# Performance work log

Measured on AMD Instinct MI355X. Metric: run time of the kernel, lower is better.

## Reference

```python
import jax, jax.numpy as jnp
import numpy as np

T_VALUES = [0.015, 0.06, 0.25, 1.0]
EPS = 1e-05
SR_OVER_HOP = 44100.0 / 512.0  # frames per second


def _s_values():
    t = np.asarray(T_VALUES, dtype=np.float32) * SR_OVER_HOP
    s = (np.sqrt(1.0 + 4.0 * t ** 2) - 1.0) / (2.0 * t ** 2)
    return jnp.asarray(s, dtype=jnp.float32)  # (n_s,)


def setup_inputs() -> dict:
    key = jax.random.key(0)
    k1, = jax.random.split(key, 1)
    B, F, T = 16, 128, 4096
    # non-negative energies (spectrogram magnitudes)
    x = jax.random.uniform(k1, (B, F, T), dtype=jnp.float32) * 10.0
    alpha_log = jnp.full((F,), float(np.log(0.8)), dtype=jnp.float32)
    delta_log = jnp.full((F,), float(np.log(10.0)), dtype=jnp.float32)
    r_log = jnp.full((F,), float(np.log(0.25)), dtype=jnp.float32)
    return {"x": x, "alpha_log": alpha_log, "delta_log": delta_log, "r_log": r_log}


def reference(x, alpha_log, delta_log, r_log):
    # x: (B, F, T)
    s = _s_values()                      # (n_s,)
    s_b = s[:, None, None]               # (n_s, 1, 1)
    B, F, T = x.shape
    n_s = s.shape[0]

    # Multi-rate EMA over time (first-order IIR), init with first frame.
    xs = jnp.moveaxis(x, -1, 0)          # (T, B, F)
    m0 = jnp.broadcast_to(xs[0][None], (n_s, B, F))

    def step(m, xt):
        m = (1.0 - s_b) * m + s_b * xt[None]  # (n_s, B, F)
        return m, m

    _, m_rest = jax.lax.scan(step, m0, xs[1:])          # (T-1, n_s, B, F)
    m_seq = jnp.concatenate([m0[None], m_rest], axis=0)  # (T, n_s, B, F)
    smoother = jnp.moveaxis(m_seq, 0, -1)                # (n_s, B, F, T)

    alpha = jnp.exp(alpha_log)[None, None, :, None]      # per band
    delta = jnp.exp(delta_log)[None, None, :, None]
    r = jnp.exp(r_log)[None, None, :, None]

    log_eps = jnp.log(jnp.asarray(EPS, dtype=x.dtype))
    smooth = jnp.exp(-alpha * (log_eps + jnp.log1p(smoother / EPS)))
    pcen = (x[None] * smooth + delta) ** r - delta ** r   # (n_s, B, F, T)
    return jnp.transpose(pcen, (1, 0, 2, 3))              # (B, n_s, F, T)
```

## Files before the change

kernel.cpp:

```cpp
#include <hip/hip_runtime.h>


#define EPS_C 1e-5f

__device__ __forceinline__ float fexp2(float v) { return __builtin_amdgcn_exp2f(v); }
__device__ __forceinline__ float flog2(float v) { return __builtin_amdgcn_logf(v); }
__device__ __forceinline__ float fpow(float a, float b) { return fexp2(b * flog2(a)); }
__device__ __forceinline__ float fexp(float v) { return fexp2(v * 1.44269504f); }

__global__ __launch_bounds__(1024)
void pcen_kernel(const float* __restrict__ x,
                 const float* __restrict__ alpha_log,
                 const float* __restrict__ delta_log,
                 const float* __restrict__ r_log,
                 float* __restrict__ out)
{
    const int row  = blockIdx.x;
    const int f    = row & 127;
    const int b    = row >> 7;
    const int tid  = threadIdx.x;
    const int lane = tid & 63;
    const int w    = tid >> 6;

    __shared__ float wq[4][16];
    __shared__ float sh_x0;

    const float4* __restrict__ xrow4 = (const float4*)(x + (size_t)row * 4096);
    float4 xv = xrow4[tid];
    if (tid == 0) sh_x0 = xv.x;

    const float Tv[4] = {0.015f, 0.06f, 0.25f, 1.0f};
    float s_arr[4], omn_arr[4];
#pragma unroll
    for (int i = 0; i < 4; ++i) {
        float t  = Tv[i] * 86.1328125f;
        float t2 = t * t;
        float s  = (__builtin_sqrtf(1.0f + 4.0f * t2) - 1.0f) / (2.0f * t2);
        s_arr[i]   = s;
        omn_arr[i] = 1.0f - s;
    }

    float qxv[4];
#pragma unroll
    for (int i = 0; i < 4; ++i) {
        const float s = s_arr[i], omn = omn_arr[i];
        float p = s * xv.x;
        p = fmaf(omn, p, s * xv.y);
        p = fmaf(omn, p, s * xv.z);
        p = fmaf(omn, p, s * xv.w);
        float q = p;
        float c = omn * omn; c = c * c;
#pragma unroll
        for (int k = 0; k < 6; ++k) {
            int d = 1 << k;
            float tsh = __shfl_up(q, d);
            if (lane >= d) q = fmaf(c, tsh, q);
            c = c * c;
        }
        float qx = __shfl_up(q, 1);
        if (lane == 0) qx = 0.0f;
        qxv[i] = qx;
        if (lane == 63) wq[i][w] = q;
    }
    __syncthreads();

    const float al = alpha_log[f], dl = delta_log[f], rl = r_log[f];
    const float nalpha  = -fexp(al);
    const float delta   =  fexp(dl);
    const float r       =  fexp(rl);
    const float delta_r =  fexp(r * dl);

    const float x0 = sh_x0;
    float4* __restrict__ out4 = (float4*)out;

#pragma unroll
    for (int i = 0; i < 4; ++i) {
        const float s = s_arr[i], omn = omn_arr[i];
        const float l2omn = flog2(omn);
        const float Dw = fexp2(256.0f * l2omn);
        float Q = x0;
        for (int v = 0; v < w; ++v) Q = fmaf(Dw, Q, wq[i][v]);
        const float dl4 = fexp2((float)(4 * lane) * l2omn);
        const float E = fmaf(dl4, Q, qxv[i]);
        float m0 = fmaf(omn, E,  s * xv.x);
        float m1 = fmaf(omn, m0, s * xv.y);
        float m2 = fmaf(omn, m1, s * xv.z);
        float m3 = fmaf(omn, m2, s * xv.w);
        float4 o;
        o.x = fpow(fmaf(xv.x, fpow(EPS_C + m0, nalpha), delta), r) - delta_r;
        o.y = fpow(fmaf(xv.y, fpow(EPS_C + m1, nalpha), delta), r) - delta_r;
        o.z = fpow(fmaf(xv.z, fpow(EPS_C + m2, nalpha), delta), r) - delta_r;
        o.w = fpow(fmaf(xv.w, fpow(EPS_C + m3, nalpha), delta), r) - delta_r;

        const size_t obase4 = ((size_t)((b * 4 + i) * 128 + f)) * 1024;
        out4[obase4 + tid] = o;
    }
}

extern "C" void kernel_launch(void* const* d_in, const int* in_sizes, int n_in,
                              void* d_out, int out_size, void* d_ws, size_t ws_size,
                              hipStream_t stream) {
    const float* x  = (const float*)d_in[0];
    const float* al = (const float*)d_in[1];
    const float* dl = (const float*)d_in[2];
    const float* rl = (const float*)d_in[3];
    float* out = (float*)d_out;
    const int rows = in_sizes[0] / 4096;
    pcen_kernel<<<rows, 1024, 0, stream>>>(x, al, dl, rl, out);
}
```

Baseline: 164.1 us.

## Process eight samples per thread with 512-thread blocks and nontemporal stores

```diff
diff --git a/kernel.cpp b/kernel.cpp
--- a/kernel.cpp
+++ b/kernel.cpp
@@ -2,13 +2,15 @@
 
 
 #define EPS_C 1e-5f
+
+typedef float vfloat4 __attribute__((ext_vector_type(4)));
 
 __device__ __forceinline__ float fexp2(float v) { return __builtin_amdgcn_exp2f(v); }
 __device__ __forceinline__ float flog2(float v) { return __builtin_amdgcn_logf(v); }
 __device__ __forceinline__ float fpow(float a, float b) { return fexp2(b * flog2(a)); }
 __device__ __forceinline__ float fexp(float v) { return fexp2(v * 1.44269504f); }
 
-__global__ __launch_bounds__(1024)
+__global__ __launch_bounds__(512)
 void pcen_kernel(const float* __restrict__ x,
                  const float* __restrict__ alpha_log,
                  const float* __restrict__ delta_log,
@@ -22,12 +24,15 @@
     const int lane = tid & 63;
     const int w    = tid >> 6;
 
-    __shared__ float wq[4][16];
+    __shared__ float wq[4][8];
     __shared__ float sh_x0;
 
-    const float4* __restrict__ xrow4 = (const float4*)(x + (size_t)row * 4096);
-    float4 xv = xrow4[tid];
-    if (tid == 0) sh_x0 = xv.x;
+    const float al = alpha_log[f], dl = delta_log[f], rl = r_log[f];
+
+    const vfloat4* __restrict__ xrow4 = (const vfloat4*)(x + (size_t)row * 4096);
+    vfloat4 xa = xrow4[2 * tid];
+    vfloat4 xb = xrow4[2 * tid + 1];
+    if (tid == 0) sh_x0 = xa.x;
 
     const float Tv[4] = {0.015f, 0.06f, 0.25f, 1.0f};
     float s_arr[4], omn_arr[4];
@@ -44,12 +49,16 @@
 #pragma unroll
     for (int i = 0; i < 4; ++i) {
         const float s = s_arr[i], omn = omn_arr[i];
-        float p = s * xv.x;
-        p = fmaf(omn, p, s * xv.y);
-        p = fmaf(omn, p, s * xv.z);
-        p = fmaf(omn, p, s * xv.w);
+        float p = s * xa.x;
+        p = fmaf(omn, p, s * xa.y);
+        p = fmaf(omn, p, s * xa.z);
+        p = fmaf(omn, p, s * xa.w);
+        p = fmaf(omn, p, s * xb.x);
+        p = fmaf(omn, p, s * xb.y);
+        p = fmaf(omn, p, s * xb.z);
+        p = fmaf(omn, p, s * xb.w);
         float q = p;
-        float c = omn * omn; c = c * c;
+        float c = omn * omn; c = c * c; c = c * c;
 #pragma unroll
         for (int k = 0; k < 6; ++k) {
             int d = 1 << k;
@@ -64,36 +73,44 @@
     }
     __syncthreads();
 
-    const float al = alpha_log[f], dl = delta_log[f], rl = r_log[f];
     const float nalpha  = -fexp(al);
     const float delta   =  fexp(dl);
     const float r       =  fexp(rl);
     const float delta_r =  fexp(r * dl);
 
     const float x0 = sh_x0;
-    float4* __restrict__ out4 = (float4*)out;
+    vfloat4* __restrict__ out4 = (vfloat4*)out;
 
 #pragma unroll
     for (int i = 0; i < 4; ++i) {
         const float s = s_arr[i], omn = omn_arr[i];
         const float l2omn = flog2(omn);
-        const float Dw = fexp2(256.0f * l2omn);
+        const float Dw = fexp2(512.0f * l2omn);
         float Q = x0;
         for (int v = 0; v < w; ++v) Q = fmaf(Dw, Q, wq[i][v]);
-        const float dl4 = fexp2((float)(4 * lane) * l2omn);
-        const float E = fmaf(dl4, Q, qxv[i]);
-        float m0 = fmaf(omn, E,  s * xv.x);
-        float m1 = fmaf(omn, m0, s * xv.y);
-        float m2 = fmaf(omn, m1, s * xv.z);
-        float m3 = fmaf(omn, m2, s * xv.w);
-        float4 o;
-        o.x = fpow(fmaf(xv.x, fpow(EPS_C + m0, nalpha), delta), r) - delta_r;
-        o.y = fpow(fmaf(xv.y, fpow(EPS_C + m1, nalpha), delta), r) - delta_r;
-        o.z = fpow(fmaf(xv.z, fpow(EPS_C + m2, nalpha), delta), r) - delta_r;
-        o.w = fpow(fmaf(xv.w, fpow(EPS_C + m3, nalpha), delta), r) - delta_r;
+        const float dl8 = fexp2((float)(8 * lane) * l2omn);
+        const float E = fmaf(dl8, Q, qxv[i]);
+        float m0 = fmaf(omn, E,  s * xa.x);
+        float m1 = fmaf(omn, m0, s * xa.y);
+        float m2 = fmaf(omn, m1, s * xa.z);
+        float m3 = fmaf(omn, m2, s * xa.w);
+        float m4 = fmaf(omn, m3, s * xb.x);
+        float m5 = fmaf(omn, m4, s * xb.y);
+        float m6 = fmaf(omn, m5, s * xb.z);
+        float m7 = fmaf(omn, m6, s * xb.w);
+        vfloat4 oa, ob;
+        oa.x = fpow(fmaf(xa.x, fpow(EPS_C + m0, nalpha), delta), r) - delta_r;
+        oa.y = fpow(fmaf(xa.y, fpow(EPS_C + m1, nalpha), delta), r) - delta_r;
+        oa.z = fpow(fmaf(xa.z, fpow(EPS_C + m2, nalpha), delta), r) - delta_r;
+        oa.w = fpow(fmaf(xa.w, fpow(EPS_C + m3, nalpha), delta), r) - delta_r;
+        ob.x = fpow(fmaf(xb.x, fpow(EPS_C + m4, nalpha), delta), r) - delta_r;
+        ob.y = fpow(fmaf(xb.y, fpow(EPS_C + m5, nalpha), delta), r) - delta_r;
+        ob.z = fpow(fmaf(xb.z, fpow(EPS_C + m6, nalpha), delta), r) - delta_r;
+        ob.w = fpow(fmaf(xb.w, fpow(EPS_C + m7, nalpha), delta), r) - delta_r;
 
         const size_t obase4 = ((size_t)((b * 4 + i) * 128 + f)) * 1024;
-        out4[obase4 + tid] = o;
+        __builtin_nontemporal_store(oa, &out4[obase4 + 2 * tid]);
+        __builtin_nontemporal_store(ob, &out4[obase4 + 2 * tid + 1]);
     }
 }
 
@@ -106,5 +123,5 @@
     const float* rl = (const float*)d_in[3];
     float* out = (float*)d_out;
     const int rows = in_sizes[0] / 4096;
-    pcen_kernel<<<rows, 1024, 0, stream>>>(x, al, dl, rl, out);
+    pcen_kernel<<<rows, 512, 0, stream>>>(x, al, dl, rl, out);
 }
```

Result: slower. 186.0 us (+13.3%).
